# Kernel optimization log

Measured on AMD Instinct MI355X. Metric: run time of the kernel, lower is better.

The kernel has to match this reference:

```python
import jax, jax.numpy as jnp
import numpy as np
import math

B, S, D, H = 4, 2048, 1024, 16
DK = D // H


def setup_inputs() -> dict:
    key = jax.random.key(0)
    ks = jax.random.split(key, 12)
    scale = 1.0 / math.sqrt(D)
    inp = {
        "x": jax.random.normal(ks[0], (B, S, D), jnp.float32),
        "q": jax.random.normal(ks[1], (B, S, D), jnp.float32),
        "k": jax.random.normal(ks[2], (B, S, D), jnp.float32),
        "v": jax.random.normal(ks[3], (B, S, D), jnp.float32),
        # causal mask: 1 = keep, 0 = masked
        "mask": jnp.tril(jnp.ones((S, S), jnp.int32))[None, None],
        "wq": jax.random.normal(ks[4], (D, D), jnp.float32) * scale,
        "bq": jnp.zeros((D,), jnp.float32),
        "wk": jax.random.normal(ks[5], (D, D), jnp.float32) * scale,
        "bk": jnp.zeros((D,), jnp.float32),
        "wv": jax.random.normal(ks[6], (D, D), jnp.float32) * scale,
        "bv": jnp.zeros((D,), jnp.float32),
        "wo": jax.random.normal(ks[7], (D, D), jnp.float32) * scale,
        "bo": jnp.zeros((D,), jnp.float32),
    }
    return inp


def _split_heads(t):  # [B,S,D] -> [B,H,S,DK]
    return t.reshape(B, S, H, DK).transpose(0, 2, 1, 3)


def reference(x, q, k, v, mask, wq, bq, wk, bk, wv, bv, wo, bo):
    # x is accepted for signature parity with the torch module but is
    # overwritten inside the original forward; it does not affect output.
    query = _split_heads(q @ wq + bq)
    key_h = _split_heads(k @ wk + bk)
    value = _split_heads(v @ wv + bv)
    # scores: [B,H,Sq,Sk]
    scores = jnp.einsum("bhqd,bhkd->bhqk", query, key_h) / math.sqrt(DK)
    scores = jnp.where(mask == 0, jnp.float32(-1e9), scores)
    attn = jax.nn.softmax(scores, axis=-1)  # dropout p=0.0 -> identity
    out = jnp.einsum("bhqk,bhkd->bhqd", attn, value)
    out = out.transpose(0, 2, 1, 3).reshape(B, S, D)
    return out @ wo + bo
```

## Files before the change

### kernel.cpp

```cpp
#include <hip/hip_runtime.h>

typedef unsigned short u16;
typedef __bf16 bf16x8 __attribute__((ext_vector_type(8)));
typedef float f32x4 __attribute__((ext_vector_type(4)));
typedef u16 u16x8 __attribute__((ext_vector_type(8)));
typedef u16 u16x4 __attribute__((ext_vector_type(4)));

static constexpr int Bb = 4, Ss = 2048, Dd = 1024, Hh = 16, DKk = 64;
static constexpr int Mg = Bb * Ss;
static constexpr int Kg = Dd;
static constexpr int Ng = Dd;

#if __has_builtin(__builtin_amdgcn_exp2f)
#define EXP2 __builtin_amdgcn_exp2f
#else
#define EXP2 exp2f
#endif

__device__ __forceinline__ u16 f2b(float f) {
    union { __bf16 h; u16 u; } c; c.h = (__bf16)f; return c.u;
}

typedef const __attribute__((address_space(1))) void gas_t;
typedef __attribute__((address_space(3))) void las_t;
__device__ __forceinline__ void gll16(const void* g, void* l) {
    __builtin_amdgcn_global_load_lds((gas_t*)g, (las_t*)l, 16, 0, 0);
}

__global__ __launch_bounds__(256) void conv3_kernel(const float* __restrict__ q,
                                                    const float* __restrict__ k,
                                                    const float* __restrict__ v,
                                                    u16* __restrict__ oq,
                                                    u16* __restrict__ ok,
                                                    u16* __restrict__ ov) {
    const size_t per = (size_t)Mg * Kg / 8;
    size_t id = (size_t)blockIdx.x * 256 + threadIdx.x;
    size_t t = id / per, off = (id % per) * 8;
    const float* src = (t == 0) ? q : (t == 1) ? k : v;
    u16* dst = (t == 0) ? oq : (t == 1) ? ok : ov;
    float4 a = *(const float4*)(src + off);
    float4 b = *(const float4*)(src + off + 4);
    u16x8 o;
    o[0] = f2b(a.x); o[1] = f2b(a.y); o[2] = f2b(a.z); o[3] = f2b(a.w);
    o[4] = f2b(b.x); o[5] = f2b(b.y); o[6] = f2b(b.z); o[7] = f2b(b.w);
    *(u16x8*)(dst + off) = o;
}

__global__ __launch_bounds__(256) void wt4_kernel(const float* w0, const float* w1,
                                                  const float* w2, const float* w3,
                                                  u16* t0, u16* t1, u16* t2, u16* t3) {
    const float* W; u16* Wt;
    switch (blockIdx.z) {
        case 0: W = w0; Wt = t0; break;
        case 1: W = w1; Wt = t1; break;
        case 2: W = w2; Wt = t2; break;
        default: W = w3; Wt = t3; break;
    }
    __shared__ __attribute__((aligned(16))) u16 T[64 * 72];
    const int k0 = blockIdx.x * 64, n0 = blockIdx.y * 64;
    const int tid = threadIdx.x;
    for (int i = 0; i < 4; ++i) {
        int flat = tid + i * 256;
        int r = flat >> 4, c4 = flat & 15;
        float4 w4 = *(const float4*)(W + (size_t)(k0 + r) * 1024 + n0 + c4 * 4);
        u16* d = &T[r * 72 + c4 * 4];
        d[0] = f2b(w4.x); d[1] = f2b(w4.y); d[2] = f2b(w4.z); d[3] = f2b(w4.w);
    }
    __syncthreads();
    for (int i = 0; i < 2; ++i) {
        int flat = tid + i * 256;
        int n = flat >> 3, c8 = flat & 7;
        u16x8 v;
        for (int jj = 0; jj < 8; ++jj) v[jj] = T[(c8 * 8 + jj) * 72 + n];
        *(u16x8*)(Wt + (size_t)(n0 + n) * 1024 + k0 + c8 * 8) = v;
    }
}

template <int MODE>
__global__ __launch_bounds__(256) void gemm_kernel(const u16* __restrict__ A,
                                                   const u16* __restrict__ Bt,
                                                   const float* __restrict__ bias,
                                                   void* __restrict__ Out,
                                                   float scale) {
    __shared__ __attribute__((aligned(16))) u16 As[128 * 32];
    __shared__ __attribute__((aligned(16))) u16 Bs[128 * 32];
    const int tid = threadIdx.x;
    const int wave = tid >> 6, lane = tid & 63;
    const int quad = lane >> 4, l15 = lane & 15;
    const int m0 = blockIdx.x * 128, n0 = blockIdx.y * 128;
    const int wm = (wave >> 1) * 64, wn = (wave & 1) * 64;
    const int rr = lane >> 2, cc = (lane & 3) * 8;

    const u16* Ag = A + (size_t)(m0 + wave * 32 + rr) * Kg + cc;
    const u16* Bg = Bt + (size_t)(n0 + wave * 32 + rr) * Kg + cc;
    u16* Asw = &As[wave * 32 * 32];
    u16* Bsw = &Bs[wave * 32 * 32];

    f32x4 acc[4][4] = {};

    for (int k0 = 0; k0 < Kg; k0 += 32) {
        __syncthreads();
        gll16(Ag + k0, Asw);
        gll16(Ag + k0 + (size_t)16 * Kg, Asw + 16 * 32);
        gll16(Bg + k0, Bsw);
        gll16(Bg + k0 + (size_t)16 * Kg, Bsw + 16 * 32);
        __syncthreads();

        bf16x8 a[4], b[4];
        for (int i = 0; i < 4; ++i)
            a[i] = *(const bf16x8*)(&As[(wm + i * 16 + l15) * 32 + quad * 8]);
        for (int j = 0; j < 4; ++j)
            b[j] = *(const bf16x8*)(&Bs[(wn + j * 16 + l15) * 32 + quad * 8]);
        for (int i = 0; i < 4; ++i)
            for (int j = 0; j < 4; ++j)
                acc[i][j] = __builtin_amdgcn_mfma_f32_16x16x32_bf16(a[i], b[j], acc[i][j], 0, 0, 0);
    }

    for (int i = 0; i < 4; ++i) {
        for (int j = 0; j < 4; ++j) {
            int col = n0 + wn + j * 16 + l15;
            float bv = bias[col];
            if (MODE == 0) {
                int h = col >> 6, dk = col & 63;
                for (int r = 0; r < 4; ++r) {
                    int row = m0 + wm + i * 16 + quad * 4 + r;
                    int bb = row >> 11, s = row & 2047;
                    ((u16*)Out)[((((size_t)bb * Hh + h) * Ss) + s) * DKk + dk] =
                        f2b((acc[i][j][r] + bv) * scale);
                }
            } else if (MODE == 2) {
                int h = col >> 6, dk = col & 63;
                int row0 = m0 + wm + i * 16 + quad * 4;
                int bb = row0 >> 11, s0 = row0 & 2047;
                u16x4 pk;
                for (int r = 0; r < 4; ++r) pk[r] = f2b(acc[i][j][r] + bv);
                *(u16x4*)((u16*)Out + (((size_t)bb * Hh + h) * DKk + dk) * Ss + s0) = pk;
            } else {
                for (int r = 0; r < 4; ++r) {
                    int row = m0 + wm + i * 16 + quad * 4 + r;
                    ((float*)Out)[(size_t)row * Ng + col] = acc[i][j][r] + bv;
                }
            }
        }
    }
}

__global__ __launch_bounds__(256) void attn_kernel(const u16* __restrict__ Qw,
                                                   const u16* __restrict__ Kw,
                                                   const u16* __restrict__ Vt,
                                                   u16* __restrict__ Ow) {
    __shared__ __attribute__((aligned(16))) u16 Qs[2 * 64 * 32];
    __shared__ __attribute__((aligned(16))) u16 Ks[2 * 64 * 32];
    __shared__ __attribute__((aligned(16))) u16 Vs[2 * 64 * 32];
    __shared__ __attribute__((aligned(16))) u16 Ps[4 * 16 * 72];

    const int idx = blockIdx.x;
    const int qt = (Ss / 64 - 1) - (idx >> 6);
    const int bh = idx & 63;
    const int q0 = qt * 64;
    const int tid = threadIdx.x, wave = tid >> 6, lane = tid & 63;
    const int quad = lane >> 4, l15 = lane & 15;
    const int rr = lane >> 2, cc = (lane & 3) * 8;

    const u16* Qb = Qw + (size_t)bh * Ss * DKk;
    const u16* Kb = Kw + (size_t)bh * Ss * DKk;
    const u16* Vb = Vt + (size_t)bh * DKk * Ss;

    for (int kc = 0; kc < 2; ++kc)
        gll16(Qb + (size_t)(q0 + wave * 16 + rr) * DKk + kc * 32 + cc,
              &Qs[kc * 2048 + wave * 16 * 32]);
    __syncthreads();
    bf16x8 aq0 = *(const bf16x8*)(&Qs[(wave * 16 + l15) * 32 + quad * 8]);
    bf16x8 aq1 = *(const bf16x8*)(&Qs[2048 + (wave * 16 + l15) * 32 + quad * 8]);

    f32x4 acc_o[4] = {};
    float m_r[4], l_r[4];
    int rowg[4];
    for (int r = 0; r < 4; ++r) {
        m_r[r] = -1e30f; l_r[r] = 0.f;
        rowg[r] = q0 + wave * 16 + quad * 4 + r;
    }
    u16* Pw = &Ps[wave * 16 * 72];

    for (int j = 0; j <= qt; ++j) {
        __syncthreads();
        for (int c = 0; c < 2; ++c) {
            gll16(Kb + (size_t)(j * 64 + wave * 16 + rr) * DKk + c * 32 + cc,
                  &Ks[c * 2048 + wave * 16 * 32]);
            gll16(Vb + (size_t)(wave * 16 + rr) * Ss + j * 64 + c * 32 + cc,
                  &Vs[c * 2048 + wave * 16 * 32]);
        }
        __syncthreads();

        f32x4 sacc[4];
        for (int ct = 0; ct < 4; ++ct) {
            bf16x8 bk0 = *(const bf16x8*)(&Ks[(ct * 16 + l15) * 32 + quad * 8]);
            bf16x8 bk1 = *(const bf16x8*)(&Ks[2048 + (ct * 16 + l15) * 32 + quad * 8]);
            f32x4 z = {};
            z = __builtin_amdgcn_mfma_f32_16x16x32_bf16(aq0, bk0, z, 0, 0, 0);
            z = __builtin_amdgcn_mfma_f32_16x16x32_bf16(aq1, bk1, z, 0, 0, 0);
            sacc[ct] = z;
        }

        if (j == qt) {
            for (int ct = 0; ct < 4; ++ct) {
                int ck = j * 64 + ct * 16 + l15;
                for (int r = 0; r < 4; ++r)
                    if (ck > rowg[r]) sacc[ct][r] = -1e30f;
            }
        }

        float mnew[4], alpha[4];
        for (int r = 0; r < 4; ++r) {
            float mx = fmaxf(fmaxf(sacc[0][r], sacc[1][r]), fmaxf(sacc[2][r], sacc[3][r]));
            for (int off = 1; off < 16; off <<= 1)
                mx = fmaxf(mx, __shfl_xor(mx, off, 64));
            mnew[r] = fmaxf(m_r[r], mx);
        }
        for (int r = 0; r < 4; ++r) {
            alpha[r] = EXP2(m_r[r] - mnew[r]);
            float sum = 0.f;
            for (int ct = 0; ct < 4; ++ct) {
                float p = EXP2(sacc[ct][r] - mnew[r]);
                sacc[ct][r] = p;
                sum += p;
            }
            for (int off = 1; off < 16; off <<= 1)
                sum += __shfl_xor(sum, off, 64);
            l_r[r] = l_r[r] * alpha[r] + sum;
            m_r[r] = mnew[r];
        }
        for (int dt = 0; dt < 4; ++dt)
            for (int r = 0; r < 4; ++r) acc_o[dt][r] *= alpha[r];

        for (int ct = 0; ct < 4; ++ct)
            for (int r = 0; r < 4; ++r)
                Pw[(quad * 4 + r) * 72 + ct * 16 + l15] = f2b(sacc[ct][r]);

        for (int sc = 0; sc < 2; ++sc) {
            bf16x8 ap = *(const bf16x8*)(&Pw[l15 * 72 + sc * 32 + quad * 8]);
            for (int dt = 0; dt < 4; ++dt) {
                bf16x8 bv = *(const bf16x8*)(&Vs[sc * 2048 + (dt * 16 + l15) * 32 + quad * 8]);
                acc_o[dt] = __builtin_amdgcn_mfma_f32_16x16x32_bf16(ap, bv, acc_o[dt], 0, 0, 0);
            }
        }
    }

    const int b = bh >> 4, h = bh & 15;
    for (int r = 0; r < 4; ++r) {
        float inv = 1.f / l_r[r];
        int s = q0 + wave * 16 + quad * 4 + r;
        for (int dt = 0; dt < 4; ++dt) {
            int dk = dt * 16 + l15;
            Ow[(((size_t)b * Ss + s) * Hh + h) * DKk + dk] = f2b(acc_o[dt][r] * inv);
        }
    }
}

extern "C" void kernel_launch(void* const* d_in, const int* in_sizes, int n_in,
                              void* d_out, int out_size, void* d_ws, size_t ws_size,
                              hipStream_t stream) {
    const float* q  = (const float*)d_in[1];
    const float* k  = (const float*)d_in[2];
    const float* v  = (const float*)d_in[3];
    const float* wq = (const float*)d_in[5];
    const float* bq = (const float*)d_in[6];
    const float* wk = (const float*)d_in[7];
    const float* bk = (const float*)d_in[8];
    const float* wv = (const float*)d_in[9];
    const float* bv = (const float*)d_in[10];
    const float* wo = (const float*)d_in[11];
    const float* bo = (const float*)d_in[12];
    float* out = (float*)d_out;

    u16* WqT = (u16*)d_ws;
    u16* WkT = WqT + 1024 * 1024;
    u16* WvT = WkT + 1024 * 1024;
    u16* WoT = WvT + 1024 * 1024;
    u16* Qc  = WoT + 1024 * 1024;
    u16* Kc  = Qc + (size_t)Mg * Kg;
    u16* Vc  = Kc + (size_t)Mg * Kg;
    u16* Qw  = Vc + (size_t)Mg * Kg;
    u16* Kw  = Qw + (size_t)Mg * Kg;
    u16* VwT = Kw + (size_t)Mg * Kg;
    u16* Ow  = Qc;

    conv3_kernel<<<dim3(3 * (Mg * Kg / 8) / 256), 256, 0, stream>>>(q, k, v, Qc, Kc, Vc);
    wt4_kernel<<<dim3(16, 16, 4), 256, 0, stream>>>(wq, wk, wv, wo, WqT, WkT, WvT, WoT);

    dim3 gg(Mg / 128, Ng / 128);
    const float qscale = 0.125f * 1.44269504f;
    gemm_kernel<0><<<gg, 256, 0, stream>>>(Qc, WqT, bq, Qw, qscale);
    gemm_kernel<0><<<gg, 256, 0, stream>>>(Kc, WkT, bk, Kw, 1.0f);
    gemm_kernel<2><<<gg, 256, 0, stream>>>(Vc, WvT, bv, VwT, 1.0f);

    attn_kernel<<<dim3(2048), 256, 0, stream>>>(Qw, Kw, VwT, Ow);

    gemm_kernel<1><<<gg, 256, 0, stream>>>(Ow, WoT, bo, out, 1.0f);
}
```

Baseline: 406.8 us.

## Transpose attention MFMA so each lane owns one query row's softmax state

Swaps the MFMA operand order in both attention matmuls so the score and output tiles are transposed, and each lane holds a single query row. Row max and sum then need only two cross-lane shuffles instead of four per row, and the running statistics shrink to scalars. It also skips the output rescale when no row's max changed, and packs the P-tile and output stores into 4-wide vector writes. The P staging buffer now reuses the Q shared-memory region, which lowers LDS use at the cost of tighter coupling between those two buffers.

```diff
diff --git a/kernel.cpp b/kernel.cpp
--- a/kernel.cpp
+++ b/kernel.cpp
@@ -149,10 +149,9 @@
                                                    const u16* __restrict__ Kw,
                                                    const u16* __restrict__ Vt,
                                                    u16* __restrict__ Ow) {
-    __shared__ __attribute__((aligned(16))) u16 Qs[2 * 64 * 32];
+    __shared__ __attribute__((aligned(16))) u16 QPs[4608];
     __shared__ __attribute__((aligned(16))) u16 Ks[2 * 64 * 32];
     __shared__ __attribute__((aligned(16))) u16 Vs[2 * 64 * 32];
-    __shared__ __attribute__((aligned(16))) u16 Ps[4 * 16 * 72];
 
     const int idx = blockIdx.x;
     const int qt = (Ss / 64 - 1) - (idx >> 6);
@@ -168,19 +167,15 @@
 
     for (int kc = 0; kc < 2; ++kc)
         gll16(Qb + (size_t)(q0 + wave * 16 + rr) * DKk + kc * 32 + cc,
-              &Qs[kc * 2048 + wave * 16 * 32]);
+              &QPs[kc * 2048 + wave * 16 * 32]);
     __syncthreads();
-    bf16x8 aq0 = *(const bf16x8*)(&Qs[(wave * 16 + l15) * 32 + quad * 8]);
-    bf16x8 aq1 = *(const bf16x8*)(&Qs[2048 + (wave * 16 + l15) * 32 + quad * 8]);
+    bf16x8 aq0 = *(const bf16x8*)(&QPs[(wave * 16 + l15) * 32 + quad * 8]);
+    bf16x8 aq1 = *(const bf16x8*)(&QPs[2048 + (wave * 16 + l15) * 32 + quad * 8]);
 
     f32x4 acc_o[4] = {};
-    float m_r[4], l_r[4];
-    int rowg[4];
-    for (int r = 0; r < 4; ++r) {
-        m_r[r] = -1e30f; l_r[r] = 0.f;
-        rowg[r] = q0 + wave * 16 + quad * 4 + r;
-    }
-    u16* Pw = &Ps[wave * 16 * 72];
+    float m_r = -1e30f, l_r = 0.f;
+    const int qrow = q0 + wave * 16 + l15;
+    u16* Pw = &QPs[wave * 16 * 72];
 
     for (int j = 0; j <= qt; ++j) {
         __syncthreads();
@@ -197,63 +192,68 @@
             bf16x8 bk0 = *(const bf16x8*)(&Ks[(ct * 16 + l15) * 32 + quad * 8]);
             bf16x8 bk1 = *(const bf16x8*)(&Ks[2048 + (ct * 16 + l15) * 32 + quad * 8]);
             f32x4 z = {};
-            z = __builtin_amdgcn_mfma_f32_16x16x32_bf16(aq0, bk0, z, 0, 0, 0);
-            z = __builtin_amdgcn_mfma_f32_16x16x32_bf16(aq1, bk1, z, 0, 0, 0);
+            z = __builtin_amdgcn_mfma_f32_16x16x32_bf16(bk0, aq0, z, 0, 0, 0);
+            z = __builtin_amdgcn_mfma_f32_16x16x32_bf16(bk1, aq1, z, 0, 0, 0);
             sacc[ct] = z;
         }
 
         if (j == qt) {
             for (int ct = 0; ct < 4; ++ct) {
-                int ck = j * 64 + ct * 16 + l15;
+                int kbase = j * 64 + ct * 16 + quad * 4;
                 for (int r = 0; r < 4; ++r)
-                    if (ck > rowg[r]) sacc[ct][r] = -1e30f;
+                    if (kbase + r > qrow) sacc[ct][r] = -1e30f;
             }
         }
 
-        float mnew[4], alpha[4];
-        for (int r = 0; r < 4; ++r) {
-            float mx = fmaxf(fmaxf(sacc[0][r], sacc[1][r]), fmaxf(sacc[2][r], sacc[3][r]));
-            for (int off = 1; off < 16; off <<= 1)
-                mx = fmaxf(mx, __shfl_xor(mx, off, 64));
-            mnew[r] = fmaxf(m_r[r], mx);
-        }
-        for (int r = 0; r < 4; ++r) {
-            alpha[r] = EXP2(m_r[r] - mnew[r]);
-            float sum = 0.f;
-            for (int ct = 0; ct < 4; ++ct) {
-                float p = EXP2(sacc[ct][r] - mnew[r]);
+        float mx = sacc[0][0];
+        for (int ct = 0; ct < 4; ++ct)
+            for (int r = 0; r < 4; ++r) mx = fmaxf(mx, sacc[ct][r]);
+        mx = fmaxf(mx, __shfl_xor(mx, 16, 64));
+        mx = fmaxf(mx, __shfl_xor(mx, 32, 64));
+        float mnew = fmaxf(m_r, mx);
+
+        float sum = 0.f;
+        for (int ct = 0; ct < 4; ++ct)
+            for (int r = 0; r < 4; ++r) {
+                float p = EXP2(sacc[ct][r] - mnew);
                 sacc[ct][r] = p;
                 sum += p;
             }
-            for (int off = 1; off < 16; off <<= 1)
-                sum += __shfl_xor(sum, off, 64);
-            l_r[r] = l_r[r] * alpha[r] + sum;
-            m_r[r] = mnew[r];
-        }
-        for (int dt = 0; dt < 4; ++dt)
-            for (int r = 0; r < 4; ++r) acc_o[dt][r] *= alpha[r];
-
-        for (int ct = 0; ct < 4; ++ct)
-            for (int r = 0; r < 4; ++r)
-                Pw[(quad * 4 + r) * 72 + ct * 16 + l15] = f2b(sacc[ct][r]);
+        sum += __shfl_xor(sum, 16, 64);
+        sum += __shfl_xor(sum, 32, 64);
+
+        bool renorm = mnew > m_r;
+        float alpha = renorm ? EXP2(m_r - mnew) : 1.0f;
+        l_r = l_r * alpha + sum;
+        m_r = mnew;
+        if (__any(renorm && m_r > -1e29f)) {
+            for (int dt = 0; dt < 4; ++dt)
+                for (int r = 0; r < 4; ++r) acc_o[dt][r] *= alpha;
+        }
+
+        for (int ct = 0; ct < 4; ++ct) {
+            u16x4 pk;
+            for (int r = 0; r < 4; ++r) pk[r] = f2b(sacc[ct][r]);
+            *(u16x4*)(&Pw[l15 * 72 + ct * 16 + quad * 4]) = pk;
+        }
 
         for (int sc = 0; sc < 2; ++sc) {
             bf16x8 ap = *(const bf16x8*)(&Pw[l15 * 72 + sc * 32 + quad * 8]);
             for (int dt = 0; dt < 4; ++dt) {
                 bf16x8 bv = *(const bf16x8*)(&Vs[sc * 2048 + (dt * 16 + l15) * 32 + quad * 8]);
-                acc_o[dt] = __builtin_amdgcn_mfma_f32_16x16x32_bf16(ap, bv, acc_o[dt], 0, 0, 0);
+                acc_o[dt] = __builtin_amdgcn_mfma_f32_16x16x32_bf16(bv, ap, acc_o[dt], 0, 0, 0);
             }
         }
     }
 
     const int b = bh >> 4, h = bh & 15;
-    for (int r = 0; r < 4; ++r) {
-        float inv = 1.f / l_r[r];
-        int s = q0 + wave * 16 + quad * 4 + r;
-        for (int dt = 0; dt < 4; ++dt) {
-            int dk = dt * 16 + l15;
-            Ow[(((size_t)b * Ss + s) * Hh + h) * DKk + dk] = f2b(acc_o[dt][r] * inv);
-        }
+    const float inv = 1.f / l_r;
+    const int s = q0 + wave * 16 + l15;
+    u16* orow = Ow + (((size_t)b * Ss + s) * Hh + h) * DKk;
+    for (int dt = 0; dt < 4; ++dt) {
+        u16x4 pk;
+        for (int r = 0; r < 4; ++r) pk[r] = f2b(acc_o[dt][r] * inv);
+        *(u16x4*)(orow + dt * 16 + quad * 4) = pk;
     }
 }
 
```

Measured after the change: 363.9 us. 1.12x faster.
